# Kernel optimization log

Measured on AMD Instinct MI355X. Metric: run time of the kernel, lower is better.

Reference implementation:

```python
import jax, jax.numpy as jnp
import numpy as np

DIM = 2048
NUM_HEADS = 32
NUM_KV_HEADS = 8
HEAD_DIM = DIM // NUM_HEADS           # 64
KV_REPEAT = NUM_HEADS // NUM_KV_HEADS  # 4
KV_DIM = HEAD_DIM * NUM_KV_HEADS      # 512
THRESHOLD = 0.05


def _init_weight(key, out_f, in_f):
    # kaiming_uniform(a=sqrt(5)) ~ U(-1/sqrt(in_f), 1/sqrt(in_f))
    bound = 1.0 / np.sqrt(in_f)
    return jax.random.uniform(key, (out_f, in_f), jnp.float32, -bound, bound)


def ternarize_ste(w):
    scale = jnp.maximum(jnp.abs(w).mean(), 1e-6)
    t = jnp.where(w > THRESHOLD * scale, 1.0,
                  jnp.where(w < -THRESHOLD * scale, -1.0, 0.0))
    return w + jax.lax.stop_gradient(t - w)


def setup_inputs() -> dict:
    key = jax.random.key(0)
    kx, kq, kk, kv, ko = jax.random.split(key, 5)
    x = jax.random.normal(kx, (2, 2048, DIM), jnp.float32)
    wq = _init_weight(kq, DIM, DIM)
    wk = _init_weight(kk, KV_DIM, DIM)
    wv = _init_weight(kv, KV_DIM, DIM)
    wo = _init_weight(ko, DIM, DIM)
    return {"x": x, "wq": wq, "wk": wk, "wv": wv, "wo": wo}


def reference(x, wq, wk, wv, wo):
    b, s, _ = x.shape
    g, r, d = NUM_KV_HEADS, KV_REPEAT, HEAD_DIM
    q = x @ ternarize_ste(wq).T   # [b,s,dim]
    k = x @ ternarize_ste(wk).T   # [b,s,kv_dim]
    v = x @ ternarize_ste(wv).T   # [b,s,kv_dim]
    # group heads as (kv_group g, repeat r) to avoid physically expanding KV
    q = q.reshape(b, s, g, r, d)
    k = k.reshape(b, s, g, d)
    v = v.reshape(b, s, g, d)
    att = jnp.einsum('bqgrd,bkgd->bgrqk', q, k) / np.sqrt(d).astype(jnp.float32)
    causal = jnp.tril(jnp.ones((s, s), dtype=bool))  # [q,k] keep lower tri
    att = jnp.where(causal, att, -jnp.inf)
    probs = jax.nn.softmax(att, axis=-1)
    out = jnp.einsum('bgrqk,bkgd->bqgrd', probs, v).reshape(b, s, DIM)
    return out @ ternarize_ste(wo).T
```

## Files before the change

kernel.cpp:

```cpp
#include <hip/hip_runtime.h>
#include <hip/hip_bf16.h>
#include <stdint.h>

#define DIMN 2048
#define KVD  512
#define NH   32
#define BATCH 2
#define SEQ  2048
#define ROWS (BATCH*SEQ)
#define NT   (SEQ/64)

typedef __attribute__((ext_vector_type(4))) float f32x4;
typedef __attribute__((ext_vector_type(8))) short bf16x8;

__device__ __forceinline__ float bf2f(short s){
  union{uint32_t u;float f;} v; v.u=((uint32_t)(uint16_t)s)<<16; return v.f;
}
__device__ __forceinline__ short f2bf_rn(float f){
  __hip_bfloat16 h = __float2bfloat16(f);
  short s; __builtin_memcpy(&s, &h, 2); return s;
}
__device__ __forceinline__ f32x4 mfma16(bf16x8 a, bf16x8 b, f32x4 c){
  return __builtin_amdgcn_mfma_f32_16x16x32_bf16(a,b,c,0,0,0);
}
__device__ __forceinline__ short ternbf(float v, float thr){
  return v > thr ? (short)0x3F80 : (v < -thr ? (short)0xBF80 : (short)0);
}
__device__ __forceinline__ void gload16(const short* g, short* l){
  __builtin_amdgcn_global_load_lds(
      (const __attribute__((address_space(1))) uint32_t*)g,
      (__attribute__((address_space(3))) uint32_t*)l, 16, 0, 0);
}

__global__ void k_abssum4(const float* __restrict__ w0, const float* __restrict__ w1,
                          const float* __restrict__ w2, const float* __restrict__ w3,
                          float* __restrict__ partial){
  __shared__ float red[256];
  const float* ptrs[4] = {w0, w1, w2, w3};
  const int ns[4] = {DIMN*DIMN, KVD*DIMN, KVD*DIMN, DIMN*DIMN};
  const int wi = blockIdx.y;
  const float* w = ptrs[wi];
  const int n = ns[wi];
  float s = 0.f;
  for (int i = blockIdx.x*256 + threadIdx.x; i < n; i += 256*gridDim.x) s += fabsf(w[i]);
  red[threadIdx.x] = s; __syncthreads();
  for (int o = 128; o > 0; o >>= 1){
    if (threadIdx.x < o) red[threadIdx.x] += red[threadIdx.x+o];
    __syncthreads();
  }
  if (threadIdx.x == 0) partial[wi*256 + blockIdx.x] = red[0];
}

__global__ void k_scales(const float* __restrict__ partial, float* __restrict__ scales){
  __shared__ float red[256];
  int t = threadIdx.x;
  const int counts[4] = {DIMN*DIMN, KVD*DIMN, KVD*DIMN, DIMN*DIMN};
  for (int wi = 0; wi < 4; wi++){
    red[t] = partial[wi*256 + t]; __syncthreads();
    for (int o = 128; o > 0; o >>= 1){
      if (t < o) red[t] += red[t+o];
      __syncthreads();
    }
    if (t == 0){
      float mean = red[0] / (float)counts[wi];
      scales[wi] = 0.05f * fmaxf(mean, 1e-6f);
    }
    __syncthreads();
  }
}

__global__ void k_prep_x(const float* __restrict__ x, short* __restrict__ hi,
                         short* __restrict__ lo){
  long i = ((long)blockIdx.x*256 + threadIdx.x)*8;
  f32x4 a = *(const f32x4*)(x+i);
  f32x4 b = *(const f32x4*)(x+i+4);
  bf16x8 h, l;
  #pragma unroll
  for (int j = 0; j < 4; j++){
    short p = f2bf_rn(a[j]); h[j]   = p; l[j]   = f2bf_rn(a[j]-bf2f(p));
    short q = f2bf_rn(b[j]); h[4+j] = q; l[4+j] = f2bf_rn(b[j]-bf2f(q));
  }
  *(bf16x8*)(hi+i) = h;
  *(bf16x8*)(lo+i) = l;
}

__global__ void k_tern4(const float* __restrict__ w0, const float* __restrict__ w1,
                        const float* __restrict__ w2, const float* __restrict__ w3,
                        short* __restrict__ o0, short* __restrict__ o1,
                        short* __restrict__ o2, short* __restrict__ o3,
                        const float* __restrict__ scales){
  const float* ws[4] = {w0, w1, w2, w3};
  short* os[4] = {o0, o1, o2, o3};
  const int ns[4] = {DIMN*DIMN, KVD*DIMN, KVD*DIMN, DIMN*DIMN};
  const int wi = blockIdx.y;
  long i = ((long)blockIdx.x*256 + threadIdx.x)*8;
  if (i >= ns[wi]) return;
  const float thr = scales[wi];
  const float* w = ws[wi];
  f32x4 a = *(const f32x4*)(w+i);
  f32x4 b = *(const f32x4*)(w+i+4);
  bf16x8 t;
  #pragma unroll
  for (int j = 0; j < 4; j++){
    t[j]   = ternbf(a[j], thr);
    t[4+j] = ternbf(b[j], thr);
  }
  *(bf16x8*)(os[wi]+i) = t;
}

template<int SPLITA, int SPLITB, int OUTF32>
__device__ __forceinline__ void gemm_core(
    const short* __restrict__ Ahg, const short* __restrict__ Xlg,
    const short* __restrict__ Bg,
    float* __restrict__ Of, short* __restrict__ Oh, short* __restrict__ Ol,
    bool writelo, int N, int K, int bn, int bm,
    short (*AhS)[64], short (*XlS)[64], short (*BsS)[64]){
  const int tid = threadIdx.x, lane = tid & 63, w = tid >> 6;
  const int wr = w >> 1, wc = w & 1;
  const int la = lane & 15, kg = lane >> 4;
  const int xrb = SPLITA ? bm : bn;
  f32x4 acc[4][4] = {};
  for (int k0 = 0; k0 < K; k0 += 64){
    #pragma unroll
    for (int j = 0; j < 4; j++){
      const int flat = (w*4 + j)*64 + lane;
      const int row = flat >> 3, c16 = (flat & 7)*8;
      short* lb = &AhS[0][0] + (w*4 + j)*512;
      gload16(Ahg + (long)(bm+row)*K + k0 + c16, lb);
    }
    if constexpr (SPLITA || SPLITB){
      #pragma unroll
      for (int j = 0; j < 4; j++){
        const int flat = (w*4 + j)*64 + lane;
        const int row = flat >> 3, c16 = (flat & 7)*8;
        short* lb = &XlS[0][0] + (w*4 + j)*512;
        gload16(Xlg + (long)(xrb+row)*K + k0 + c16, lb);
      }
    }
    #pragma unroll
    for (int j = 0; j < 4; j++){
      const int flat = (w*4 + j)*64 + lane;
      const int row = flat >> 3, c16 = (flat & 7)*8;
      short* lb = &BsS[0][0] + (w*4 + j)*512;
      gload16(Bg + (long)(bn+row)*K + k0 + c16, lb);
    }
    __syncthreads();
    #pragma unroll
    for (int ks = 0; ks < 2; ks++){
      bf16x8 af[4], bfr[4];
      #pragma unroll
      for (int mi = 0; mi < 4; mi++)
        af[mi] = *(bf16x8*)&AhS[wr*64 + mi*16 + la][ks*32 + kg*8];
      #pragma unroll
      for (int ni = 0; ni < 4; ni++)
        bfr[ni] = *(bf16x8*)&BsS[wc*64 + ni*16 + la][ks*32 + kg*8];
      #pragma unroll
      for (int mi = 0; mi < 4; mi++)
        #pragma unroll
        for (int ni = 0; ni < 4; ni++)
          acc[mi][ni] = mfma16(af[mi], bfr[ni], acc[mi][ni]);
      if constexpr (SPLITA){
        bf16x8 alf[4];
        #pragma unroll
        for (int mi = 0; mi < 4; mi++)
          alf[mi] = *(bf16x8*)&XlS[wr*64 + mi*16 + la][ks*32 + kg*8];
        #pragma unroll
        for (int mi = 0; mi < 4; mi++)
          #pragma unroll
          for (int ni = 0; ni < 4; ni++)
            acc[mi][ni] = mfma16(alf[mi], bfr[ni], acc[mi][ni]);
      }
      if constexpr (SPLITB){
        bf16x8 blf[4];
        #pragma unroll
        for (int ni = 0; ni < 4; ni++)
          blf[ni] = *(bf16x8*)&XlS[wc*64 + ni*16 + la][ks*32 + kg*8];
        #pragma unroll
        for (int mi = 0; mi < 4; mi++)
          #pragma unroll
          for (int ni = 0; ni < 4; ni++)
            acc[mi][ni] = mfma16(af[mi], blf[ni], acc[mi][ni]);
      }
    }
    __syncthreads();
  }
  #pragma unroll
  for (int mi = 0; mi < 4; mi++)
    #pragma unroll
    for (int ni = 0; ni < 4; ni++)
      #pragma unroll
      for (int rr = 0; rr < 4; rr++){
        long row = bm + wr*64 + mi*16 + kg*4 + rr;
        long col = bn + wc*64 + ni*16 + la;
        float v = acc[mi][ni][rr];
        if constexpr (OUTF32){
          Of[row*(long)N + col] = v;
        } else {
          short hb = f2bf_rn(v);
          Oh[row*(long)N + col] = hb;
          if (writelo)
            Ol[row*(long)N + col] = f2bf_rn(v - bf2f(hb));
        }
      }
}

__global__ __launch_bounds__(256) void k_gemm_q(
    const short* __restrict__ Ahg, const short* __restrict__ Alg,
    const short* __restrict__ Bg, short* __restrict__ Oh, short* __restrict__ Ol,
    int N, int K){
  __shared__ short S0[128][64];
  __shared__ short S1[128][64];
  __shared__ short S2[128][64];
  gemm_core<1,0,0>(Ahg, Alg, Bg, nullptr, Oh, Ol, true, N, K,
                   blockIdx.x*128, blockIdx.y*128, S0, S1, S2);
}

__global__ __launch_bounds__(256) void k_gemm_kvt(
    const short* __restrict__ xhi, const short* __restrict__ xlo,
    const short* __restrict__ wkT, const short* __restrict__ wvT,
    short* __restrict__ KOh, short* __restrict__ KOl, short* __restrict__ VT,
    int K){
  __shared__ short S0[128][64];
  __shared__ short S1[128][64];
  __shared__ short S2[128][64];
  if (blockIdx.z == 0){
    gemm_core<1,0,0>(xhi, xlo, wkT, nullptr, KOh, KOl, true, KVD, K,
                     blockIdx.x*128, blockIdx.y*128, S0, S1, S2);
  } else {
    gemm_core<0,1,0>(wvT, xlo, xhi, nullptr, VT, nullptr, false, ROWS, K,
                     blockIdx.y*128, blockIdx.x*128, S0, S1, S2);
  }
}

__global__ __launch_bounds__(256) void k_gemm_o(
    const short* __restrict__ Ahg, const short* __restrict__ Bg,
    float* __restrict__ Of, int N, int K){
  __shared__ short S0[128][64];
  __shared__ short S2[128][64];
  gemm_core<0,0,1>(Ahg, nullptr, Bg, Of, nullptr, nullptr, false, N, K,
                   blockIdx.x*128, blockIdx.y*128, S0, nullptr, S2);
}

__global__ __launch_bounds__(256) void k_attn(
    const short* __restrict__ qhi, const short* __restrict__ qlo,
    const short* __restrict__ khi, const short* __restrict__ klo,
    const short* __restrict__ vT, short* __restrict__ attout){
  __shared__ short Kh[64][68];
  __shared__ short Kl[64][68];
  __shared__ short Vt[64][68];
  __shared__ short P[64][68];
  const float SC = 0.125f * 1.44269504f;
  const int qp = blockIdx.x, h = blockIdx.y, b = blockIdx.z;
  const int g = h >> 2;
  const int tid = threadIdx.x, w = tid >> 6, lane = tid & 63;
  const int la = lane & 15, kg = lane >> 4;
  const int trow = tid >> 2, tcol = (tid & 3) * 16;

  for (int phase = 0; phase < 2; phase++){
    const int qt = phase ? (NT - 1 - qp) : qp;
    const int qbase = qt*64;

    bf16x8 qh[2], ql[2];
    {
      long qrow = (long)(b*SEQ + qbase + w*16 + la);
      #pragma unroll
      for (int ks = 0; ks < 2; ks++){
        long off = qrow*DIMN + h*64 + ks*32 + kg*8;
        qh[ks] = *(const bf16x8*)(qhi + off);
        ql[ks] = *(const bf16x8*)(qlo + off);
      }
    }
    f32x4 Oacc[4] = {};
    float m[4], l[4];
    #pragma unroll
    for (int r = 0; r < 4; r++){ m[r] = -INFINITY; l[r] = 0.f; }

    for (int kt = 0; kt <= qt; kt++){
      __syncthreads();
      {
        const short* ksrc  = khi + (long)(b*SEQ + kt*64 + trow)*KVD + g*64 + tcol;
        const short* klsrc = klo + (long)(b*SEQ + kt*64 + trow)*KVD + g*64 + tcol;
        const short* vsrc  = vT  + (long)(g*64 + trow)*ROWS + b*SEQ + kt*64 + tcol;
        *(bf16x8*)&Kh[trow][tcol]   = *(const bf16x8*)ksrc;
        *(bf16x8*)&Kh[trow][tcol+8] = *(const bf16x8*)(ksrc + 8);
        *(bf16x8*)&Kl[trow][tcol]   = *(const bf16x8*)klsrc;
        *(bf16x8*)&Kl[trow][tcol+8] = *(const bf16x8*)(klsrc + 8);
        *(bf16x8*)&Vt[trow][tcol]   = *(const bf16x8*)vsrc;
        *(bf16x8*)&Vt[trow][tcol+8] = *(const bf16x8*)(vsrc + 8);
      }
      __syncthreads();

      f32x4 s[4];
      __builtin_amdgcn_s_setprio(1);
      #pragma unroll
      for (int ni = 0; ni < 4; ni++){
        f32x4 a = {0.f,0.f,0.f,0.f};
        #pragma unroll
        for (int ks = 0; ks < 2; ks++){
          bf16x8 kh = *(bf16x8*)&Kh[ni*16 + la][ks*32 + kg*8];
          bf16x8 kl = *(bf16x8*)&Kl[ni*16 + la][ks*32 + kg*8];
          a = mfma16(qh[ks], kh, a);
          a = mfma16(ql[ks], kh, a);
          a = mfma16(qh[ks], kl, a);
        }
        s[ni] = a;
      }
      __builtin_amdgcn_s_setprio(0);

      const bool lastTile = (kt == qt);
      #pragma unroll
      for (int ni = 0; ni < 4; ni++)
        #pragma unroll
        for (int r = 0; r < 4; r++){
          float v = s[ni][r] * SC;
          if (lastTile){
            int kc = kt*64 + ni*16 + la;
            int qr = qbase + w*16 + kg*4 + r;
            if (kc > qr) v = -INFINITY;
          }
          s[ni][r] = v;
        }

      float pm[4];
      #pragma unroll
      for (int r = 0; r < 4; r++){
        float v = fmaxf(fmaxf(s[0][r], s[1][r]), fmaxf(s[2][r], s[3][r]));
        for (int o = 1; o < 16; o <<= 1) v = fmaxf(v, __shfl_xor(v, o, 64));
        pm[r] = v;
      }
      float gr = -INFINITY;
      #pragma unroll
      for (int r = 0; r < 4; r++) gr = fmaxf(gr, pm[r] - m[r]);
      if (!__all(gr <= 8.0f)){
        #pragma unroll
        for (int r = 0; r < 4; r++){
          float mn = fmaxf(m[r], pm[r]);
          float ef = exp2f(m[r] - mn);
          m[r] = mn; l[r] *= ef;
          #pragma unroll
          for (int d = 0; d < 4; d++) Oacc[d][r] *= ef;
        }
      }
      #pragma unroll
      for (int r = 0; r < 4; r++){
        float rs = 0.f;
        #pragma unroll
        for (int ni = 0; ni < 4; ni++){
          float p = exp2f(s[ni][r] - m[r]);
          s[ni][r] = p;
          rs += p;
        }
        for (int o = 1; o < 16; o <<= 1) rs += __shfl_xor(rs, o, 64);
        l[r] += rs;
      }

      #pragma unroll
      for (int ni = 0; ni < 4; ni++)
        #pragma unroll
        for (int r = 0; r < 4; r++)
          P[w*16 + kg*4 + r][ni*16 + la] = f2bf_rn(s[ni][r]);

      __builtin_amdgcn_s_setprio(1);
      #pragma unroll
      for (int ks = 0; ks < 2; ks++){
        bf16x8 pa = *(bf16x8*)&P[w*16 + la][ks*32 + kg*8];
        #pragma unroll
        for (int d = 0; d < 4; d++){
          bf16x8 vb = *(bf16x8*)&Vt[d*16 + la][ks*32 + kg*8];
          Oacc[d] = mfma16(pa, vb, Oacc[d]);
        }
      }
      __builtin_amdgcn_s_setprio(0);
    }

    #pragma unroll
    for (int d = 0; d < 4; d++)
      #pragma unroll
      for (int r = 0; r < 4; r++){
        float v = Oacc[d][r] / l[r];
        long row = (long)(b*SEQ + qbase + w*16 + kg*4 + r);
        attout[row*DIMN + h*64 + d*16 + la] = f2bf_rn(v);
      }
    __syncthreads();
  }
}

extern "C" void kernel_launch(void* const* d_in, const int* in_sizes, int n_in,
                              void* d_out, int out_size, void* d_ws, size_t ws_size,
                              hipStream_t stream){
  const float* x  = (const float*)d_in[0];
  const float* wq = (const float*)d_in[1];
  const float* wk = (const float*)d_in[2];
  const float* wv = (const float*)d_in[3];
  const float* wo = (const float*)d_in[4];
  float* out = (float*)d_out;
  char* ws = (char*)d_ws;

  const size_t SZ_QD = (size_t)ROWS*DIMN*2;
  const size_t SZ_KD = (size_t)ROWS*KVD*2;
  const size_t SZ_WQ = (size_t)DIMN*DIMN*2;
  const size_t SZ_WK = (size_t)KVD*DIMN*2;
  const size_t NEED = 65536 + 2*SZ_QD + 2*SZ_WQ + 2*SZ_WK + 2*SZ_QD + 3*SZ_KD;
  if (ws_size < NEED) return;

  float* scales   = (float*)ws;
  float* partials = (float*)(ws + 1024);
  size_t off = 65536;
  auto alloc = [&](size_t bytes)->char*{
    char* p = ws + off; off += (bytes + 255) & ~(size_t)255; return p;
  };
  short* xhi = (short*)alloc(SZ_QD);
  short* xlo = (short*)alloc(SZ_QD);
  short* wqT = (short*)alloc(SZ_WQ);
  short* wkT = (short*)alloc(SZ_WK);
  short* wvT = (short*)alloc(SZ_WK);
  short* woT = (short*)alloc(SZ_WQ);
  short* qhib = (short*)alloc(SZ_QD);
  short* qlob = (short*)alloc(SZ_QD);
  short* khib = (short*)alloc(SZ_KD);
  short* klob = (short*)alloc(SZ_KD);
  short* vTb  = (short*)alloc(SZ_KD);
  short* atto = xhi;

  {
    dim3 g(256, 4);
    k_abssum4<<<g,256,0,stream>>>(wq, wk, wv, wo, partials);
  }
  k_scales<<<1,256,0,stream>>>(partials, scales);

  {
    dim3 g(2048, 4);
    k_tern4<<<g,256,0,stream>>>(wq, wk, wv, wo, wqT, wkT, wvT, woT, scales);
  }
  k_prep_x<<<4096,256,0,stream>>>(x, xhi, xlo);

  {
    dim3 g(DIMN/128, ROWS/128);
    k_gemm_q<<<g,256,0,stream>>>(xhi, xlo, wqT, qhib, qlob, DIMN, DIMN);
  }
  {
    dim3 g(KVD/128, ROWS/128, 2);
    k_gemm_kvt<<<g,256,0,stream>>>(xhi, xlo, wkT, wvT, khib, klob, vTb, DIMN);
  }

  {
    dim3 g(NT/2, NH, BATCH);
    k_attn<<<g,256,0,stream>>>(qhib, qlob, khib, klob, vTb, atto);
  }

  {
    dim3 g(DIMN/128, ROWS/128);
    k_gemm_o<<<g,256,0,stream>>>(atto, woT, out, DIMN, DIMN);
  }
}
```

Before: 513.3 us.

## Merge Q/K/V projection launches and make softmax rescale unconditional with fast exp2

The Q projection and the K/V(transposed) projection kernels are merged into one launch with a z dimension of 3. Blocks beyond the KV width exit early, which removes one launch and the serialization between the two GEMMs. In attention, the lazy rescale (skipped when the max grows by at most 8) is replaced by an unconditional per-tile rescale, and exp2f is swapped for the hardware exp2 builtin. This trims the wave-vote branch and exp cost, but adds multiplies on the O accumulator every tile. The merged grid also launches a large number of blocks that exit immediately.

```diff
diff --git a/kernel.cpp b/kernel.cpp
--- a/kernel.cpp
+++ b/kernel.cpp
@@ -25,6 +25,13 @@
 }
 __device__ __forceinline__ short ternbf(float v, float thr){
   return v > thr ? (short)0x3F80 : (v < -thr ? (short)0xBF80 : (short)0);
+}
+__device__ __forceinline__ float exp2_fast(float x){
+#if __has_builtin(__builtin_amdgcn_exp2f)
+  return __builtin_amdgcn_exp2f(x);
+#else
+  return __expf(x * 0.69314718056f);
+#endif
 }
 __device__ __forceinline__ void gload16(const short* g, short* l){
   __builtin_amdgcn_global_load_lds(
@@ -204,30 +211,26 @@
       }
 }
 
-__global__ __launch_bounds__(256) void k_gemm_q(
-    const short* __restrict__ Ahg, const short* __restrict__ Alg,
-    const short* __restrict__ Bg, short* __restrict__ Oh, short* __restrict__ Ol,
-    int N, int K){
+__global__ __launch_bounds__(256) void k_gemm_qkvt(
+    const short* __restrict__ xhi, const short* __restrict__ xlo,
+    const short* __restrict__ wqT, const short* __restrict__ wkT,
+    const short* __restrict__ wvT,
+    short* __restrict__ Qh, short* __restrict__ Ql,
+    short* __restrict__ KOh, short* __restrict__ KOl, short* __restrict__ VT){
   __shared__ short S0[128][64];
   __shared__ short S1[128][64];
   __shared__ short S2[128][64];
-  gemm_core<1,0,0>(Ahg, Alg, Bg, nullptr, Oh, Ol, true, N, K,
-                   blockIdx.x*128, blockIdx.y*128, S0, S1, S2);
-}
-
-__global__ __launch_bounds__(256) void k_gemm_kvt(
-    const short* __restrict__ xhi, const short* __restrict__ xlo,
-    const short* __restrict__ wkT, const short* __restrict__ wvT,
-    short* __restrict__ KOh, short* __restrict__ KOl, short* __restrict__ VT,
-    int K){
-  __shared__ short S0[128][64];
-  __shared__ short S1[128][64];
-  __shared__ short S2[128][64];
-  if (blockIdx.z == 0){
-    gemm_core<1,0,0>(xhi, xlo, wkT, nullptr, KOh, KOl, true, KVD, K,
+  const int z = blockIdx.z;
+  if (z == 0){
+    gemm_core<1,0,0>(xhi, xlo, wqT, nullptr, Qh, Ql, true, DIMN, DIMN,
+                     blockIdx.x*128, blockIdx.y*128, S0, S1, S2);
+  } else if (z == 1){
+    if (blockIdx.x >= KVD/128) return;
+    gemm_core<1,0,0>(xhi, xlo, wkT, nullptr, KOh, KOl, true, KVD, DIMN,
                      blockIdx.x*128, blockIdx.y*128, S0, S1, S2);
   } else {
-    gemm_core<0,1,0>(wvT, xlo, xhi, nullptr, VT, nullptr, false, ROWS, K,
+    if (blockIdx.x >= KVD/128) return;
+    gemm_core<0,1,0>(wvT, xlo, xhi, nullptr, VT, nullptr, false, ROWS, DIMN,
                      blockIdx.y*128, blockIdx.x*128, S0, S1, S2);
   }
 }
@@ -321,38 +324,31 @@
           s[ni][r] = v;
         }
 
-      float pm[4];
+      float ef[4];
       #pragma unroll
       for (int r = 0; r < 4; r++){
         float v = fmaxf(fmaxf(s[0][r], s[1][r]), fmaxf(s[2][r], s[3][r]));
         for (int o = 1; o < 16; o <<= 1) v = fmaxf(v, __shfl_xor(v, o, 64));
-        pm[r] = v;
-      }
-      float gr = -INFINITY;
-      #pragma unroll
-      for (int r = 0; r < 4; r++) gr = fmaxf(gr, pm[r] - m[r]);
-      if (!__all(gr <= 8.0f)){
-        #pragma unroll
-        for (int r = 0; r < 4; r++){
-          float mn = fmaxf(m[r], pm[r]);
-          float ef = exp2f(m[r] - mn);
-          m[r] = mn; l[r] *= ef;
-          #pragma unroll
-          for (int d = 0; d < 4; d++) Oacc[d][r] *= ef;
-        }
+        float mn = fmaxf(m[r], v);
+        ef[r] = exp2_fast(m[r] - mn);
+        m[r] = mn;
       }
       #pragma unroll
       for (int r = 0; r < 4; r++){
         float rs = 0.f;
         #pragma unroll
         for (int ni = 0; ni < 4; ni++){
-          float p = exp2f(s[ni][r] - m[r]);
+          float p = exp2_fast(s[ni][r] - m[r]);
           s[ni][r] = p;
           rs += p;
         }
         for (int o = 1; o < 16; o <<= 1) rs += __shfl_xor(rs, o, 64);
-        l[r] += rs;
-      }
+        l[r] = l[r]*ef[r] + rs;
+      }
+      #pragma unroll
+      for (int d = 0; d < 4; d++)
+        #pragma unroll
+        for (int r = 0; r < 4; r++) Oacc[d][r] *= ef[r];
 
       #pragma unroll
       for (int ni = 0; ni < 4; ni++)
@@ -435,12 +431,9 @@
   k_prep_x<<<4096,256,0,stream>>>(x, xhi, xlo);
 
   {
-    dim3 g(DIMN/128, ROWS/128);
-    k_gemm_q<<<g,256,0,stream>>>(xhi, xlo, wqT, qhib, qlob, DIMN, DIMN);
-  }
-  {
-    dim3 g(KVD/128, ROWS/128, 2);
-    k_gemm_kvt<<<g,256,0,stream>>>(xhi, xlo, wkT, wvT, khib, klob, vTb, DIMN);
+    dim3 g(DIMN/128, ROWS/128, 3);
+    k_gemm_qkvt<<<g,256,0,stream>>>(xhi, xlo, wqT, wkT, wvT,
+                                    qhib, qlob, khib, klob, vTb);
   }
 
   {
```

Result: slower. 559.1 us (+8.9%).
